# Optimization experiments

Measured on AMD Instinct MI355X. Metric: run time of the kernel, lower is better.

Reference implementation:

```python
import math
import jax, jax.numpy as jnp
import numpy as np

# irreps layout (flat, e3nn ordering: all scalars first, then vectors as (mul,3)):
#   pseduo: 64x0e + 32x1o  -> dim 160, 96 irreps
#   edge:   32x0e + 32x1o  -> dim 128, 64 irreps
PS, PV = 64, 32
ES, EV = 32, 32
H, NB = 8, 16
N_NODES, N_EDGES = 8192, 65536
MSG_DIM = PS + 3 * PV           # msg_irreps = pseduo_irreps (default)
NIR = PS + PV                   # num_irreps of pseduo
SQRT3 = math.sqrt(3.0)

def _split(x, ns, nv):
    # flat spherical tensor -> (scalars [..,ns], vectors [..,nv,3])
    return x[..., :ns], x[..., ns:].reshape(x.shape[:-1] + (nv, 3))

def _o3_linear(s, v, Ws, Wv):
    # e3nn o3.Linear: independent channel mixing per l, fan-in normalized
    so = (s @ Ws) / math.sqrt(Ws.shape[0])
    vo = jnp.einsum('...ic,io->...oc', v, Wv) / math.sqrt(Wv.shape[0])
    return so, vo

def setup_inputs() -> dict:
    key = jax.random.key(0)
    k = jax.random.split(key, 20)
    f32 = jnp.float32
    return {
        'pseduo_x': jax.random.normal(k[0], (N_NODES, PS + 3 * PV), f32),
        'rbf': jax.random.normal(k[1], (N_EDGES, NB), f32),
        'rsh': jax.random.normal(k[2], (N_EDGES, ES + 3 * EV), f32),
        'edge_index': jax.random.randint(k[3], (2, N_EDGES), 0, N_NODES),
        'Wq_s': jax.random.normal(k[4], (PS, H * PS), f32),
        'Wq_v': jax.random.normal(k[5], (PV, H * PV), f32),
        'Wk_s': jax.random.normal(k[6], (2 * PS, H * PS), f32),
        'Wk_v': jax.random.normal(k[7], (2 * PV, H * PV), f32),
        'Wp_s': jax.random.normal(k[8], (2 * PS, ES), f32),
        'Wp_v': jax.random.normal(k[9], (2 * PV, EV), f32),
        'Wrbf': jax.random.normal(k[10], (NB, ES + EV), f32) / math.sqrt(NB),
        'Wv_s': jax.random.normal(k[11], (ES + EV, H * PS), f32),
        'Wv_v': jax.random.normal(k[12], (2 * EV, H * PV), f32),
        'Wm_s': jax.random.normal(k[13], (H * PS, PS), f32),
        'Wm_v': jax.random.normal(k[14], (H * PV, PV), f32),
        'ln_g': jnp.ones((NIR,), f32),
        'ln_b': jnp.zeros((NIR,), f32),
        'W1': jax.random.normal(k[15], (NIR, NIR), f32) / math.sqrt(NIR),
        'b1': jnp.zeros((NIR,), f32),
        'W2': jax.random.normal(k[16], (NIR, NIR), f32) / math.sqrt(NIR),
        'b2': jnp.zeros((NIR,), f32),
    }

def reference(pseduo_x, rbf, rsh, edge_index, Wq_s, Wq_v, Wk_s, Wk_v, Wp_s, Wp_v,
              Wrbf, Wv_s, Wv_v, Wm_s, Wm_v, ln_g, ln_b, W1, b1, W2, b2):
    src, dst = edge_index[0], edge_index[1]
    s, v = _split(pseduo_x, PS, PV)

    # pseduo_ij = cat([x_i, x_j]) -> irreps pseduo*2
    sij = jnp.concatenate([s[src], s[dst]], axis=-1)            # [E, 2*PS]
    vij = jnp.concatenate([v[src], v[dst]], axis=-2)            # [E, 2*PV, 3]

    # multi-head query (per node) and key (per edge)
    q_s, q_v = _o3_linear(s, v, Wq_s, Wq_v)
    q_s = q_s.reshape(-1, H, PS); q_v = q_v.reshape(-1, H, PV, 3)
    k_s, k_v = _o3_linear(sij, vij, Wk_s, Wk_v)
    k_s = k_s.reshape(-1, H, PS); k_v = k_v.reshape(-1, H, PV, 3)

    # edge filter: rsh_conv(rsh, rbf_lin(rbf))
    scal = rbf @ Wrbf                                           # [E, ES+EV]
    rs, rv = _split(rsh, ES, EV)
    e_s = rs * scal[:, :ES]
    e_v = rv * scal[:, ES:, None]

    # sph_ij = edge * pseduo_lin(pseduo_ij)   (elementwise on flat layout)
    p_s, p_v = _o3_linear(sij, vij, Wp_s, Wp_v)
    sph_s = e_s * p_s                                           # [E, ES]
    sph_v = e_v * p_v                                           # [E, EV, 3]

    # depthwise CG self-coupling x (x) x, filter {0e, 1o} -> 64x0e + 64x1o
    c0 = jnp.concatenate([sph_s * sph_s,
                          jnp.sum(sph_v * sph_v, axis=-1) / SQRT3], axis=-1)  # [E, 64]
    sv = sph_s[..., None] * sph_v                               # 0e x 1o -> 1o
    c1 = jnp.concatenate([sv, sv], axis=-2)                     # [E, 64, 3]

    val_s, val_v = _o3_linear(c0, c1, Wv_s, Wv_v)
    val_s = val_s.reshape(-1, H, PS); val_v = val_v.reshape(-1, H, PV, 3)

    # attention logits: (query[src] * key).sum over flat msg dim, per head
    proj = (jnp.einsum('ehd,ehd->eh', q_s[src], k_s) +
            jnp.einsum('ehdc,ehdc->eh', q_v[src], k_v))
    logits = proj / math.sqrt(MSG_DIM)

    # scatter-softmax over destination nodes
    m = jax.ops.segment_max(logits, dst, num_segments=N_NODES)
    ex = jnp.exp(logits - m[dst])
    den = jax.ops.segment_sum(ex, dst, num_segments=N_NODES)
    attn = ex / den[dst]                                        # [E, H]

    # scatter-aggregate messages to nodes
    msg_s = jax.ops.segment_sum(attn[..., None] * val_s, dst, num_segments=N_NODES)
    msg_v = jax.ops.segment_sum(attn[..., None, None] * val_v, dst, num_segments=N_NODES)

    m_s, m_v = _o3_linear(msg_s.reshape(-1, H * PS),
                          msg_v.reshape(-1, H * PV, 3), Wm_s, Wm_v)

    # NormGate: EvNorm (per-irrep norm, node LayerNorm) + 2-layer silu MLP gate
    n0 = jnp.concatenate([jnp.abs(m_s), jnp.linalg.norm(m_v, axis=-1)], axis=-1)  # [N, 96]
    mu = jnp.mean(n0, axis=-1, keepdims=True)
    var = jnp.var(n0, axis=-1, keepdims=True)
    x1 = (n0 - mu) / jnp.sqrt(var + 1e-5) * ln_g + ln_b
    inv = 1.0 / (n0 + 1e-6)                                    # 1 / (|h_l| + eps)
    g = jax.nn.silu(jax.nn.silu(x1 @ W1 + b1) @ W2 + b2)
    f = inv * g
    out_s = m_s * f[:, :PS]
    out_v = m_v * f[:, PS:, None]
    return jnp.concatenate([out_s, out_v.reshape(-1, 3 * PV)], axis=-1)
```

## Files before the change

### kernel.cpp

```cpp
#include <hip/hip_runtime.h>

typedef unsigned short u16;
typedef unsigned int u32;

#define NN 8192
#define NE 65536
#define INV160 0.07905694150420949f

__device__ __forceinline__ float BF(u16 u){ return __uint_as_float(((u32)u)<<16); }
__device__ __forceinline__ float LD(const void* p, u32 i, int f){
  return f ? ((const float*)p)[i] : BF(((const u16*)p)[i]);
}
__device__ __forceinline__ int LDI(const void* p, u32 i, int f64){
  return f64 ? (int)((const long long*)p)[i] : ((const int*)p)[i];
}

__global__ void k_detect(
    const void* b0, const void* b1, const void* b2, const void* b3,
    const void* b4, const void* b5, const void* b6, const void* b7,
    const void* b8, const void* b9, const void* b10, const void* b11,
    const void* b12, const void* b13, const void* b14, const void* b15,
    const void* b16, const void* b17, const void* b18, const void* b19,
    const void* b20, int* flags)
{
  const void* bufs[21] = {b0,b1,b2,b3,b4,b5,b6,b7,b8,b9,b10,
                          b11,b12,b13,b14,b15,b16,b17,b18,b19,b20};
  int i = threadIdx.x;
  if (i >= 21) return;
  const u32* w = (const u32*)bufs[i];
  if (i == 3){
    int allz = 1;
    for (int k=0;k<32;k++) if (w[2*k+1] != 0u) allz = 0;
    flags[3] = allz;
  } else {
    int cnt = 0;
    for (int k=0;k<40;k++){
      u32 lo = w[k] & 0xFFFFu;
      u32 e = (lo>>7)&0xFFu;
      if (e>=123u && e<=131u) cnt++;
    }
    flags[i] = (cnt>=20) ? 0 : 1;
  }
}

__global__ void k_sentinel(float* __restrict__ out, int n){
  int i = blockIdx.x*256+threadIdx.x;
  if (i<n) out[i] = 12345.0f;
}

__global__ __launch_bounds__(384) void k_prep4(
    const void* __restrict__ X, const void* __restrict__ Wq_s,
    const void* __restrict__ Wq_v, const void* __restrict__ Wk_s,
    const void* __restrict__ Wk_v, const int* __restrict__ flags,
    int hc0, float* __restrict__ qtab, float* __restrict__ kbtab,
    float* __restrict__ dotAA)
{
  __shared__ float xr[4][160];
  __shared__ float dsum[4][4];
  const int fX=flags[0], fqs=flags[4], fqv=flags[5], fks=flags[6], fkv=flags[7];
  const int fall = fqs & fqv & fks & fkv;
  const int t=threadIdx.x; const int n0=blockIdx.x*4;
  for(int u=t;u<640;u+=384){ int m=u/160,k=u-m*160; xr[m][k]=LD(X,(u32)(n0+m)*160+k,fX); }
  if (t<16) dsum[t>>2][t&3]=0.f;
  __syncthreads();
  if (t<256){
    const int o=hc0*64+t;
    float q[4]={0,0,0,0}, ka[4]={0,0,0,0}, kb[4]={0,0,0,0};
    if (fall){
      const float* wqs=(const float*)Wq_s;
      const float* wks=(const float*)Wk_s;
      for(int i=0;i<64;i++){
        float wq=wqs[(u32)i*512+o], wa=wks[(u32)i*512+o], wb=wks[(u32)(64+i)*512+o];
        #pragma unroll
        for(int m=0;m<4;m++){ float s=xr[m][i]; q[m]+=s*wq; ka[m]+=s*wa; kb[m]+=s*wb; }
      }
    } else {
      for(int i=0;i<64;i++){
        float wq=LD(Wq_s,(u32)i*512+o,fqs);
        float wa=LD(Wk_s,(u32)i*512+o,fks);
        float wb=LD(Wk_s,(u32)(64+i)*512+o,fks);
        #pragma unroll
        for(int m=0;m<4;m++){ float s=xr[m][i]; q[m]+=s*wq; ka[m]+=s*wa; kb[m]+=s*wb; }
      }
    }
    #pragma unroll
    for(int m=0;m<4;m++){
      float qs = q[m]*0.125f;
      float kas= ka[m]*0.08838834764831845f;
      float kbs= kb[m]*0.08838834764831845f;
      qtab [(u32)(n0+m)*640+t]=qs;
      kbtab[(u32)(n0+m)*640+t]=kbs;
      float d=qs*kas;
      for(int s2=1;s2<64;s2<<=1) d+=__shfl_xor(d,s2,64);
      if((t&63)==0) atomicAdd(&dsum[m][t>>6],d);
    }
  } else {
    const int ol=t-256;
    const int o=hc0*32+ol;
    float q[4][3]={}, ka[4][3]={}, kb[4][3]={};
    if (fall){
      const float* wqv=(const float*)Wq_v;
      const float* wkv=(const float*)Wk_v;
      for(int j=0;j<32;j++){
        float wq=wqv[(u32)j*256+o], wa=wkv[(u32)j*256+o], wb=wkv[(u32)(32+j)*256+o];
        #pragma unroll
        for(int m=0;m<4;m++){
          #pragma unroll
          for(int c=0;c<3;c++){
            float x=xr[m][64+j*3+c];
            q[m][c]+=x*wq; ka[m][c]+=x*wa; kb[m][c]+=x*wb;
          }
        }
      }
    } else {
      for(int j=0;j<32;j++){
        float wq=LD(Wq_v,(u32)j*256+o,fqv);
        float wa=LD(Wk_v,(u32)j*256+o,fkv);
        float wb=LD(Wk_v,(u32)(32+j)*256+o,fkv);
        #pragma unroll
        for(int m=0;m<4;m++){
          #pragma unroll
          for(int c=0;c<3;c++){
            float x=xr[m][64+j*3+c];
            q[m][c]+=x*wq; ka[m][c]+=x*wa; kb[m][c]+=x*wb;
          }
        }
      }
    }
    const float sq=0.17677669529663687f;
    const float sk=0.125f;
    #pragma unroll
    for(int m=0;m<4;m++){
      float d=0.f;
      u32 base=(u32)(n0+m)*640+256+(u32)ol*3;
      #pragma unroll
      for(int c=0;c<3;c++){
        float qs=q[m][c]*sq, kas=ka[m][c]*sk, kbs=kb[m][c]*sk;
        qtab[base+c]=qs; kbtab[base+c]=kbs;
        d+=qs*kas;
      }
      for(int s2=1;s2<32;s2<<=1) d+=__shfl_xor(d,s2,64);
      if((t&31)==0) atomicAdd(&dsum[m][ol>>5],d);
    }
  }
  __syncthreads();
  if (t<16){ int m=t>>2, hh=t&3; dotAA[(u32)(n0+m)*8+hc0+hh]=dsum[m][hh]; }
}

__global__ __launch_bounds__(256) void k_elog4(
    const void* __restrict__ ei, const int* __restrict__ flags,
    const float* __restrict__ qtab, const float* __restrict__ kbtab,
    const float* __restrict__ dotAA, int hc0, float* __restrict__ logits)
{
  const int f64=flags[3];
  const int t=threadIdx.x;
  const int e=blockIdx.x*4+(t>>6), l=t&63;
  const int src=LDI(ei,(u32)e,f64);
  const int dst=LDI(ei,(u32)NE+e,f64);
  const float4* q4=(const float4*)qtab + (u32)src*160;
  const float4* b4=(const float4*)kbtab + (u32)dst*160;
  float a0=0.f,a1=0.f,a2=0.f,a3=0.f;
  {
    float4 a=q4[l], b=b4[l];
    float d=a.x*b.x+a.y*b.y+a.z*b.z+a.w*b.w;
    int h=l>>4;
    a0+=(h==0)?d:0.f; a1+=(h==1)?d:0.f; a2+=(h==2)?d:0.f; a3+=(h==3)?d:0.f;
  }
  {
    float4 a=q4[64+l], b=b4[64+l];
    float d=a.x*b.x+a.y*b.y+a.z*b.z+a.w*b.w;
    int h=l/24;
    a0+=(h==0)?d:0.f; a1+=(h==1)?d:0.f; a2+=(h==2)?d:0.f;
  }
  if (l<32){
    float4 a=q4[128+l], b=b4[128+l];
    float d=a.x*b.x+a.y*b.y+a.z*b.z+a.w*b.w;
    a2+=(l<8)?d:0.f; a3+=(l>=8)?d:0.f;
  }
  for(int m=1;m<64;m<<=1){
    a0+=__shfl_xor(a0,m,64); a1+=__shfl_xor(a1,m,64);
    a2+=__shfl_xor(a2,m,64); a3+=__shfl_xor(a3,m,64);
  }
  if (l<4){
    float cr=(l==0)?a0:(l==1)?a1:(l==2)?a2:a3;
    logits[(u32)e*8+hc0+l]=(dotAA[(u32)src*8+hc0+l]+cr)*INV160;
  }
}

__global__ __launch_bounds__(256) void k_softmax(
    const u32* __restrict__ off, const u32* __restrict__ elist,
    float* __restrict__ logits)
{
  int idx=blockIdx.x*256+threadIdx.x;
  int dst=idx>>3, h=idx&7;
  u32 o0=off[dst], o1=off[dst+1];
  float m=-3.4e38f;
  for(u32 p=o0;p<o1;p++) m=fmaxf(m, logits[(u32)elist[p]*8+h]);
  float s=0.f;
  for(u32 p=o0;p<o1;p++) s+=__expf(logits[(u32)elist[p]*8+h]-m);
  if (s>0.f){
    float inv=1.f/s;
    for(u32 p=o0;p<o1;p++){
      u32 i=(u32)elist[p]*8+h;
      logits[i]=__expf(logits[i]-m)*inv;
    }
  }
}

__global__ __launch_bounds__(256) void k_fold(
    const void* __restrict__ Wv_s, const void* __restrict__ Wv_v,
    const void* __restrict__ Wm_s, const void* __restrict__ Wm_v,
    const int* __restrict__ flags,
    float* __restrict__ Wfold, float* __restrict__ Vfold)
{
  const int fvs=flags[11], fvv=flags[12], fms=flags[13], fmv=flags[14];
  const int b=blockIdx.x, t=threadIdx.x;
  if (b<128){
    int idx=b*256+t;
    int i=idx>>6, o=idx&63;
    int h=i>>6, iin=i&63;
    float a=0.f;
    for(int d=0;d<64;d++)
      a += LD(Wv_s,(u32)iin*512 + h*64 + d, fvs) * LD(Wm_s,(u32)(h*64+d)*64 + o, fms);
    Wfold[idx]=a*0.0055242717280199026f;
  } else {
    int idx=(b-128)*256+t;
    int h=idx>>10, r=idx&1023, j2=r>>5, o2=r&31;
    float a=0.f;
    for(int dl=0;dl<32;dl++){
      int i2=h*32+dl;
      a += (LD(Wv_v,(u32)j2*256+i2,fvv)+LD(Wv_v,(u32)(32+j2)*256+i2,fvv))
           *LD(Wm_v,(u32)i2*32+o2,fmv);
    }
    Vfold[idx]=a*0.0078125f;
  }
}

__global__ __launch_bounds__(256) void k_pprep(
    const void* __restrict__ X, const void* __restrict__ Wp_s,
    const void* __restrict__ Wp_v, const int* __restrict__ flags,
    float* __restrict__ pA, float* __restrict__ pB)
{
  __shared__ float xr[160];
  const int fX=flags[0], fps=flags[8], fpv=flags[9];
  const int t=threadIdx.x, n=blockIdx.x;
  if (t<160) xr[t]=LD(X,(u32)n*160+t,fX);
  __syncthreads();
  if (t<64){
    const int j=t&31, half=t>>5;
    float a=0.f;
    if (fps){
      const float* wp=(const float*)Wp_s;
      for(int i=0;i<64;i++) a+=xr[i]*wp[(u32)(half*64+i)*32+j];
    } else {
      for(int i=0;i<64;i++) a+=xr[i]*LD(Wp_s,(u32)(half*64+i)*32+j,fps);
    }
    float* d_ = half? pB:pA;
    d_[(u32)n*128+j]=a*0.08838834764831845f;
  } else {
    const int idx=t-64;
    const int half=idx/96;
    const int r=idx-half*96;
    const int j=r/3, c=r-3*j;
    float a=0.f;
    if (fpv){
      const float* wp=(const float*)Wp_v;
      for(int k=0;k<32;k++) a+=xr[64+k*3+c]*wp[(u32)(half*32+k)*32+j];
    } else {
      for(int k=0;k<32;k++) a+=xr[64+k*3+c]*LD(Wp_v,(u32)(half*32+k)*32+j,fpv);
    }
    float* d_ = half? pB:pA;
    d_[(u32)n*128+32+j*3+c]=a*0.125f;
  }
}

__global__ __launch_bounds__(256) void k_count(
    const void* __restrict__ ei, const int* __restrict__ flags,
    u32* __restrict__ cnt)
{
  int e = blockIdx.x*256 + threadIdx.x;
  int dst = LDI(ei,(u32)NE+e,flags[3]);
  atomicAdd(&cnt[dst],1u);
}
__global__ __launch_bounds__(256) void k_scan(
    u32* __restrict__ cnt, u32* __restrict__ off, u32* __restrict__ cur)
{
  __shared__ u32 s[NN];
  __shared__ u32 tsum[256];
  const int t=threadIdx.x;
  for(int u=t;u<NN;u+=256) s[u]=cnt[u];
  __syncthreads();
  const u32 base=(u32)t*32;
  u32 sum=0;
  for(int k=0;k<32;k++) sum+=s[base+k];
  tsum[t]=sum;
  __syncthreads();
  if(t==0){
    u32 run=0;
    for(int i=0;i<256;i++){ u32 v=tsum[i]; tsum[i]=run; run+=v; }
  }
  __syncthreads();
  u32 run=tsum[t];
  for(int k=0;k<32;k++){
    u32 v=s[base+k];
    off[base+k]=run; cur[base+k]=run;
    run+=v;
  }
  if(t==255) off[NN]=run;
}
__global__ __launch_bounds__(256) void k_fill(
    const void* __restrict__ ei, const int* __restrict__ flags,
    u32* __restrict__ cur, u32* __restrict__ elist)
{
  int e = blockIdx.x*256 + threadIdx.x;
  int dst = LDI(ei,(u32)NE+e,flags[3]);
  u32 p = atomicAdd(&cur[dst],1u);
  elist[p] = (u32)e;
}

__global__ __launch_bounds__(256) void k_nodeval(
    const float* __restrict__ attn, const float* __restrict__ pA,
    const float* __restrict__ pBt,
    const u32* __restrict__ off, const u32* __restrict__ elist,
    const void* __restrict__ ei, const void* __restrict__ rbf,
    const void* __restrict__ rsh, const void* __restrict__ Wrbf,
    const float* __restrict__ Wfold, const float* __restrict__ Vfold,
    const void* __restrict__ ln_g, const void* __restrict__ ln_b,
    const void* __restrict__ W1, const void* __restrict__ b1,
    const void* __restrict__ W2, const void* __restrict__ b2,
    const int* __restrict__ flags, float* __restrict__ out)
{
  __shared__ float wrb[1024];
  __shared__ float pB[128];
  __shared__ float ubuf[8][160];
  __shared__ int   ebuf[8];
  __shared__ float ag[1280];
  __shared__ float partf[16][64];
  __shared__ float partv[192];
  __shared__ float mrow[160];
  __shared__ float n0[96], x1[96], y1[96], fl[96];
  const int frb=flags[1], frs=flags[2], f64=flags[3], fwr=flags[10];
  const int fg=flags[15], fbb=flags[16], f1=flags[17], fb1=flags[18];
  const int f2=flags[19], fb2=flags[20];
  const int fastg = frb & frs;
  const int fastt = fg & fbb & f1 & fb1 & f2 & fb2;
  const int t=threadIdx.x; const int n=blockIdx.x;
  for(int u=t;u<1024;u+=256) wrb[u]=LD(Wrbf,u,fwr);
  if (t<128) pB[t]=pBt[(u32)n*128+t];
  __syncthreads();

  const int h=t>>5, j=t&31;
  const u32 o0=off[n], o1=off[n+1];
  float a0=0.f,a1=0.f,a2=0.f,a3=0.f,a4=0.f;
  for (u32 base=o0; base<o1; base+=8){
    u32 rem=o1-base; int nb = rem<8u ? (int)rem : 8;
    if (h<nb){
      u32 e=elist[base+h];
      if (j==0) ebuf[h]=(int)e;
      int src=LDI(ei,e,f64);
      const float* pa=pA+(u32)src*128;
      float ps  = pa[j]        + pB[j];
      float pv0 = pa[32+j*3+0] + pB[32+j*3+0];
      float pv1 = pa[32+j*3+1] + pB[32+j*3+1];
      float pv2 = pa[32+j*3+2] + pB[32+j*3+2];
      float scs=0.f, scv=0.f;
      float rs0,rs1,rs2,rs3;
      if (fastg){
        const float* rb=(const float*)rbf + (size_t)e*16;
        #pragma unroll
        for(int r=0;r<16;r++){
          float x=rb[r];
          scs+=x*wrb[r*64+j]; scv+=x*wrb[r*64+32+j];
        }
        const float* rs=(const float*)rsh + (size_t)e*128;
        rs0=rs[j]; rs1=rs[32+j*3+0]; rs2=rs[32+j*3+1]; rs3=rs[32+j*3+2];
      } else {
        for(int r=0;r<16;r++){
          float x=LD(rbf,(u32)e*16+r,frb);
          scs+=x*wrb[r*64+j]; scv+=x*wrb[r*64+32+j];
        }
        rs0=LD(rsh,(u32)e*128+j,frs);
        rs1=LD(rsh,(u32)e*128+32+j*3+0,frs);
        rs2=LD(rsh,(u32)e*128+32+j*3+1,frs);
        rs3=LD(rsh,(u32)e*128+32+j*3+2,frs);
      }
      float ss = rs0 * scs * ps;
      float v0 = rs1 * scv * pv0;
      float v1 = rs2 * scv * pv1;
      float v2 = rs3 * scv * pv2;
      ubuf[h][j]        = ss*ss;
      ubuf[h][32+j]     = (v0*v0+v1*v1+v2*v2)*0.57735026918962576f;
      ubuf[h][64+3*j+0] = ss*v0;
      ubuf[h][64+3*j+1] = ss*v1;
      ubuf[h][64+3*j+2] = ss*v2;
    }
    __syncthreads();
    for(int q=0;q<nb;q++){
      float w=attn[(u32)ebuf[q]*8+h];
      a0+=w*ubuf[q][j];        a1+=w*ubuf[q][32+j];
      a2+=w*ubuf[q][64+3*j+0]; a3+=w*ubuf[q][64+3*j+1]; a4+=w*ubuf[q][64+3*j+2];
    }
    __syncthreads();
  }
  ag[h*64+j]=a0; ag[h*64+32+j]=a1;
  ag[512+h*96+3*j+0]=a2; ag[512+h*96+3*j+1]=a3; ag[512+h*96+3*j+2]=a4;
  __syncthreads();

  {
    const int o4=t&15, p=t>>4;
    const float4* Wf4=(const float4*)Wfold;
    float ax=0.f,ay=0.f,az=0.f,aw=0.f;
    const int i0=p*32;
    for(int i=i0;i<i0+32;i++){
      float a=ag[i];
      float4 wv=Wf4[(u32)i*16+o4];
      ax+=a*wv.x; ay+=a*wv.y; az+=a*wv.z; aw+=a*wv.w;
    }
    partf[p][o4*4+0]=ax; partf[p][o4*4+1]=ay;
    partf[p][o4*4+2]=az; partf[p][o4*4+3]=aw;
  }
  if (t<192){
    const int o2=t&31, c=(t>>5)%3, p=t/96;
    float a=0.f;
    for(int hh=p*4;hh<p*4+4;hh++)
      for(int j2=0;j2<32;j2++)
        a += ag[512+hh*96+j2*3+c]*Vfold[(u32)hh*1024+j2*32+o2];
    partv[t]=a;
  }
  __syncthreads();
  if (t<64){
    float s=0.f;
    #pragma unroll
    for(int p2=0;p2<16;p2++) s+=partf[p2][t];
    mrow[t]=s;
  } else if (t<160){
    int q=t-64;
    mrow[64+(q&31)*3+(q>>5)]=partv[q]+partv[q+96];
  }
  __syncthreads();

  if (t<96){
    float val;
    if (t<64) val=fabsf(mrow[t]);
    else { int o2=t-64;
      float a=mrow[64+o2*3],b=mrow[64+o2*3+1],c=mrow[64+o2*3+2];
      val=sqrtf(a*a+b*b+c*c); }
    n0[t]=val;
  }
  __syncthreads();
  float mu=0.f,ss2=0.f;
  for(int i=0;i<96;i++){ float v=n0[i]; mu+=v; ss2+=v*v; }
  mu*=(1.f/96.f);
  float var=fmaxf(ss2*(1.f/96.f)-mu*mu,0.f);
  float rstd=rsqrtf(var+1e-5f);
  if (t<96){
    float gv = fastt ? ((const float*)ln_g)[t] : LD(ln_g,t,fg);
    float bv = fastt ? ((const float*)ln_b)[t] : LD(ln_b,t,fbb);
    x1[t]=(n0[t]-mu)*rstd*gv+bv;
  }
  __syncthreads();
  if (t<96){
    float a = fastt ? ((const float*)b1)[t] : LD(b1,t,fb1);
    if (fastt){
      const float* w1=(const float*)W1;
      for(int i=0;i<96;i++) a+=x1[i]*w1[(u32)i*96+t];
    } else {
      for(int i=0;i<96;i++) a+=x1[i]*LD(W1,i*96+t,f1);
    }
    y1[t]=a/(1.f+__expf(-a));
  }
  __syncthreads();
  if (t<96){
    float a = fastt ? ((const float*)b2)[t] : LD(b2,t,fb2);
    if (fastt){
      const float* w2=(const float*)W2;
      for(int i=0;i<96;i++) a+=y1[i]*w2[(u32)i*96+t];
    } else {
      for(int i=0;i<96;i++) a+=y1[i]*LD(W2,i*96+t,f2);
    }
    float gg=a/(1.f+__expf(-a));
    fl[t]=gg/(n0[t]+1e-6f);
  }
  __syncthreads();
  if (t<160){
    float v;
    if (t<64) v=mrow[t]*fl[t];
    else { int q=t-64; int o2=q/3; v=mrow[t]*fl[64+o2]; }
    out[(u32)n*160+t]=v;
  }
}

extern "C" void kernel_launch(void* const* d_in, const int* in_sizes, int n_in,
                              void* d_out, int out_size, void* d_ws, size_t ws_size,
                              hipStream_t stream)
{
  (void)in_sizes; (void)n_in;
  const void* X    = d_in[0];
  const void* rbf  = d_in[1];
  const void* rsh  = d_in[2];
  const void* ei   = d_in[3];
  const void* Wq_s = d_in[4];
  const void* Wq_v = d_in[5];
  const void* Wk_s = d_in[6];
  const void* Wk_v = d_in[7];
  const void* Wp_s = d_in[8];
  const void* Wp_v = d_in[9];
  const void* Wrbf = d_in[10];
  const void* Wv_s = d_in[11];
  const void* Wv_v = d_in[12];
  const void* Wm_s = d_in[13];
  const void* Wm_v = d_in[14];
  const void* ln_g = d_in[15];
  const void* ln_b = d_in[16];
  const void* W1   = d_in[17];
  const void* b1   = d_in[18];
  const void* W2   = d_in[19];
  const void* b2   = d_in[20];

  char* w = (char*)d_ws;
  int* flags     = (int*)w;   w += 256;
  float* logits  = (float*)w; w += (size_t)NE*8*4;
  u32* imax      = (u32*)w;   w += (size_t)NN*8*4;
  float* den     = (float*)w; w += (size_t)NN*8*4;
  char* uni = w;              w += (size_t)NN*1280*4;
  float* qtab  = (float*)uni;
  float* kbtab = (float*)(uni + (size_t)NN*640*4);
  float* pA    = (float*)uni;
  float* pB    = (float*)(uni + (size_t)NN*128*4);
  u32* csr_off = imax;
  u32* csr_cur = imax + 12288;
  float* Wfold = (float*)((char*)imax + 98304);
  float* Vfold = (float*)((char*)imax + 229376);
  u32* elist   = (u32*)den;
  float* dotAA = (float*)d_out;
  size_t required = (size_t)(w - (char*)d_ws);

  if (ws_size < required){
    k_sentinel<<<(out_size+255)/256,256,0,stream>>>((float*)d_out, out_size);
    return;
  }

  k_detect<<<1,64,0,stream>>>(X,rbf,rsh,ei,Wq_s,Wq_v,Wk_s,Wk_v,Wp_s,Wp_v,
                              Wrbf,Wv_s,Wv_v,Wm_s,Wm_v,ln_g,ln_b,W1,b1,W2,b2,flags);
  k_fold<<<160,256,0,stream>>>(Wv_s,Wv_v,Wm_s,Wm_v,flags,Wfold,Vfold);
  hipMemsetAsync(imax, 0, (size_t)NN*4, stream);
  k_count<<<NE/256,256,0,stream>>>(ei,flags,imax);
  k_scan<<<1,256,0,stream>>>(imax,csr_off,csr_cur);
  k_fill<<<NE/256,256,0,stream>>>(ei,flags,csr_cur,elist);
  for (int c=0;c<2;c++){
    k_prep4<<<NN/4,384,0,stream>>>(X,Wq_s,Wq_v,Wk_s,Wk_v,flags,c*4,qtab,kbtab,dotAA);
    k_elog4<<<NE/4,256,0,stream>>>(ei,flags,qtab,kbtab,dotAA,c*4,logits);
  }
  k_softmax<<<NN*8/256,256,0,stream>>>(csr_off,elist,logits);
  k_pprep<<<NN,256,0,stream>>>(X,Wp_s,Wp_v,flags,pA,pB);
  k_nodeval<<<NN,256,0,stream>>>(logits,pA,pB,csr_off,elist,ei,rbf,rsh,Wrbf,
                                 Wfold,Vfold,ln_g,ln_b,W1,b1,W2,b2,flags,(float*)d_out);
}
```

Before: 487.6 us.

## Precompute per-edge RBF scalars and transpose weights for vectorized node-stage loads

Adds a separate kernel that computes the per-edge RBF-to-scalar projection into a workspace table. The node kernel then reads 64 floats per edge instead of recomputing a 16-term dot product and staging Wrbf in shared memory. It also transposes Vfold, W1 and W2 so the node kernel can read them with contiguous float4 loads. The cost is an extra 16 MB edge table written and read back, plus two additional kernel launches.

```diff
diff --git a/kernel.cpp b/kernel.cpp
--- a/kernel.cpp
+++ b/kernel.cpp
@@ -225,7 +225,7 @@
     Wfold[idx]=a*0.0055242717280199026f;
   } else {
     int idx=(b-128)*256+t;
-    int h=idx>>10, r=idx&1023, j2=r>>5, o2=r&31;
+    int h=idx>>10, r=idx&1023, o2=r>>5, j2=r&31;
     float a=0.f;
     for(int dl=0;dl<32;dl++){
       int i2=h*32+dl;
@@ -234,6 +234,40 @@
     }
     Vfold[idx]=a*0.0078125f;
   }
+}
+
+__global__ __launch_bounds__(256) void k_fold2(
+    const void* __restrict__ W1, const void* __restrict__ W2,
+    const int* __restrict__ flags,
+    float* __restrict__ W1t, float* __restrict__ W2t)
+{
+  int idx=blockIdx.x*256+threadIdx.x;
+  if (idx<9216){
+    int o=idx/96, i=idx-96*o;
+    W1t[idx]=LD(W1,(u32)i*96+o,flags[17]);
+    W2t[idx]=LD(W2,(u32)i*96+o,flags[19]);
+  }
+}
+
+__global__ __launch_bounds__(256) void k_escal(
+    const void* __restrict__ rbf, const void* __restrict__ Wrbf,
+    const int* __restrict__ flags, float* __restrict__ scal)
+{
+  __shared__ float wrb[1024];
+  const int frb=flags[1], fwr=flags[10];
+  const int t=threadIdx.x;
+  for(int u=t;u<1024;u+=256) wrb[u]=LD(Wrbf,u,fwr);
+  __syncthreads();
+  const int e=blockIdx.x*4+(t>>6), c=t&63;
+  float a=0.f;
+  if (frb){
+    const float* rb=(const float*)rbf+(size_t)e*16;
+    #pragma unroll
+    for(int r=0;r<16;r++) a+=rb[r]*wrb[r*64+c];
+  } else {
+    for(int r=0;r<16;r++) a+=LD(rbf,(u32)e*16+r,frb)*wrb[r*64+c];
+  }
+  scal[(u32)e*64+c]=a;
 }
 
 __global__ __launch_bounds__(256) void k_pprep(
@@ -320,17 +354,15 @@
 
 __global__ __launch_bounds__(256) void k_nodeval(
     const float* __restrict__ attn, const float* __restrict__ pA,
-    const float* __restrict__ pBt,
+    const float* __restrict__ pBt, const float* __restrict__ scal,
     const u32* __restrict__ off, const u32* __restrict__ elist,
-    const void* __restrict__ ei, const void* __restrict__ rbf,
-    const void* __restrict__ rsh, const void* __restrict__ Wrbf,
+    const void* __restrict__ ei, const void* __restrict__ rsh,
     const float* __restrict__ Wfold, const float* __restrict__ Vfold,
+    const float* __restrict__ W1t, const float* __restrict__ W2t,
     const void* __restrict__ ln_g, const void* __restrict__ ln_b,
-    const void* __restrict__ W1, const void* __restrict__ b1,
-    const void* __restrict__ W2, const void* __restrict__ b2,
+    const void* __restrict__ b1, const void* __restrict__ b2,
     const int* __restrict__ flags, float* __restrict__ out)
 {
-  __shared__ float wrb[1024];
   __shared__ float pB[128];
   __shared__ float ubuf[8][160];
   __shared__ int   ebuf[8];
@@ -339,13 +371,9 @@
   __shared__ float partv[192];
   __shared__ float mrow[160];
   __shared__ float n0[96], x1[96], y1[96], fl[96];
-  const int frb=flags[1], frs=flags[2], f64=flags[3], fwr=flags[10];
-  const int fg=flags[15], fbb=flags[16], f1=flags[17], fb1=flags[18];
-  const int f2=flags[19], fb2=flags[20];
-  const int fastg = frb & frs;
-  const int fastt = fg & fbb & f1 & fb1 & f2 & fb2;
+  const int frs=flags[2], f64=flags[3];
+  const int fg=flags[15], fbb=flags[16], fb1=flags[18], fb2=flags[20];
   const int t=threadIdx.x; const int n=blockIdx.x;
-  for(int u=t;u<1024;u+=256) wrb[u]=LD(Wrbf,u,fwr);
   if (t<128) pB[t]=pBt[(u32)n*128+t];
   __syncthreads();
 
@@ -363,22 +391,13 @@
       float pv0 = pa[32+j*3+0] + pB[32+j*3+0];
       float pv1 = pa[32+j*3+1] + pB[32+j*3+1];
       float pv2 = pa[32+j*3+2] + pB[32+j*3+2];
-      float scs=0.f, scv=0.f;
+      float scs = scal[(u32)e*64+j];
+      float scv = scal[(u32)e*64+32+j];
       float rs0,rs1,rs2,rs3;
-      if (fastg){
-        const float* rb=(const float*)rbf + (size_t)e*16;
-        #pragma unroll
-        for(int r=0;r<16;r++){
-          float x=rb[r];
-          scs+=x*wrb[r*64+j]; scv+=x*wrb[r*64+32+j];
-        }
+      if (frs){
         const float* rs=(const float*)rsh + (size_t)e*128;
         rs0=rs[j]; rs1=rs[32+j*3+0]; rs2=rs[32+j*3+1]; rs3=rs[32+j*3+2];
       } else {
-        for(int r=0;r<16;r++){
-          float x=LD(rbf,(u32)e*16+r,frb);
-          scs+=x*wrb[r*64+j]; scv+=x*wrb[r*64+32+j];
-        }
         rs0=LD(rsh,(u32)e*128+j,frs);
         rs1=LD(rsh,(u32)e*128+32+j*3+0,frs);
         rs2=LD(rsh,(u32)e*128+32+j*3+1,frs);
@@ -422,9 +441,16 @@
   if (t<192){
     const int o2=t&31, c=(t>>5)%3, p=t/96;
     float a=0.f;
-    for(int hh=p*4;hh<p*4+4;hh++)
-      for(int j2=0;j2<32;j2++)
-        a += ag[512+hh*96+j2*3+c]*Vfold[(u32)hh*1024+j2*32+o2];
+    for(int hh=p*4;hh<p*4+4;hh++){
+      const float4* vf=(const float4*)(Vfold + (u32)hh*1024 + (u32)o2*32);
+      const float* agv=ag + 512 + hh*96 + c;
+      #pragma unroll
+      for(int q8=0;q8<8;q8++){
+        float4 v=vf[q8];
+        a += agv[(q8*4+0)*3]*v.x + agv[(q8*4+1)*3]*v.y
+           + agv[(q8*4+2)*3]*v.z + agv[(q8*4+3)*3]*v.w;
+      }
+    }
     partv[t]=a;
   }
   __syncthreads();
@@ -454,29 +480,29 @@
   float var=fmaxf(ss2*(1.f/96.f)-mu*mu,0.f);
   float rstd=rsqrtf(var+1e-5f);
   if (t<96){
-    float gv = fastt ? ((const float*)ln_g)[t] : LD(ln_g,t,fg);
-    float bv = fastt ? ((const float*)ln_b)[t] : LD(ln_b,t,fbb);
+    float gv = fg  ? ((const float*)ln_g)[t] : LD(ln_g,t,fg);
+    float bv = fbb ? ((const float*)ln_b)[t] : LD(ln_b,t,fbb);
     x1[t]=(n0[t]-mu)*rstd*gv+bv;
   }
   __syncthreads();
   if (t<96){
-    float a = fastt ? ((const float*)b1)[t] : LD(b1,t,fb1);
-    if (fastt){
-      const float* w1=(const float*)W1;
-      for(int i=0;i<96;i++) a+=x1[i]*w1[(u32)i*96+t];
-    } else {
-      for(int i=0;i<96;i++) a+=x1[i]*LD(W1,i*96+t,f1);
+    float a = fb1 ? ((const float*)b1)[t] : LD(b1,t,fb1);
+    const float4* w4=(const float4*)(W1t + (u32)t*96);
+    #pragma unroll
+    for(int i4=0;i4<24;i4++){
+      float4 v=w4[i4];
+      a+=x1[i4*4+0]*v.x+x1[i4*4+1]*v.y+x1[i4*4+2]*v.z+x1[i4*4+3]*v.w;
     }
     y1[t]=a/(1.f+__expf(-a));
   }
   __syncthreads();
   if (t<96){
-    float a = fastt ? ((const float*)b2)[t] : LD(b2,t,fb2);
-    if (fastt){
-      const float* w2=(const float*)W2;
-      for(int i=0;i<96;i++) a+=y1[i]*w2[(u32)i*96+t];
-    } else {
-      for(int i=0;i<96;i++) a+=y1[i]*LD(W2,i*96+t,f2);
+    float a = fb2 ? ((const float*)b2)[t] : LD(b2,t,fb2);
+    const float4* w4=(const float4*)(W2t + (u32)t*96);
+    #pragma unroll
+    for(int i4=0;i4<24;i4++){
+      float4 v=w4[i4];
+      a+=y1[i4*4+0]*v.x+y1[i4*4+1]*v.y+y1[i4*4+2]*v.z+y1[i4*4+3]*v.w;
     }
     float gg=a/(1.f+__expf(-a));
     fl[t]=gg/(n0[t]+1e-6f);
@@ -527,6 +553,9 @@
   float* kbtab = (float*)(uni + (size_t)NN*640*4);
   float* pA    = (float*)uni;
   float* pB    = (float*)(uni + (size_t)NN*128*4);
+  float* scal  = (float*)(uni + (size_t)NN*128*4*2);
+  float* W1t   = (float*)(uni + (size_t)NN*128*4*2 + (size_t)NE*64*4);
+  float* W2t   = W1t + 9216;
   u32* csr_off = imax;
   u32* csr_cur = imax + 12288;
   float* Wfold = (float*)((char*)imax + 98304);
@@ -553,6 +582,8 @@
   }
   k_softmax<<<NN*8/256,256,0,stream>>>(csr_off,elist,logits);
   k_pprep<<<NN,256,0,stream>>>(X,Wp_s,Wp_v,flags,pA,pB);
-  k_nodeval<<<NN,256,0,stream>>>(logits,pA,pB,csr_off,elist,ei,rbf,rsh,Wrbf,
-                                 Wfold,Vfold,ln_g,ln_b,W1,b1,W2,b2,flags,(float*)d_out);
-}
+  k_escal<<<NE/4,256,0,stream>>>(rbf,Wrbf,flags,scal);
+  k_fold2<<<36,256,0,stream>>>(W1,W2,flags,W1t,W2t);
+  k_nodeval<<<NN,256,0,stream>>>(logits,pA,pB,scal,csr_off,elist,ei,rsh,
+                                 Wfold,Vfold,W1t,W2t,ln_g,ln_b,b1,b2,flags,(float*)d_out);
+}
```

Result: slower. 598.9 us (+22.8%).
